# Performance work log

Measured on AMD Instinct MI355X. Metric: run time of the kernel, lower is better.

Reference implementation:

```python
import jax, jax.numpy as jnp
import numpy as np

N_TASK = 50000
N_PROC = 256
N_EDGES = 800000
EMB = 64
HEADS = 4
NLAYERS = 3
EDIM = 8
TDIM = 16
PDIM = 8
NGRAPHS = 8


def setup_inputs():
    key = jax.random.key(0)
    ks = jax.random.split(key, 30)

    def nrm(k, shape, fan_in):
        return jax.random.normal(k, shape, jnp.float32) / np.float32(np.sqrt(fan_in))

    inp = {}
    inp["x_task"] = jax.random.normal(ks[0], (N_TASK, TDIM), jnp.float32)
    inp["x_proc"] = jax.random.normal(ks[1], (N_PROC, PDIM), jnp.float32)
    inp["edge_index"] = jax.random.randint(ks[2], (2, N_EDGES), 0, N_TASK, dtype=jnp.int32)
    inp["edge_attr"] = jax.random.uniform(ks[3], (N_EDGES, EDIM), jnp.float32)
    inp["task_batch"] = jnp.sort(jax.random.randint(ks[4], (N_TASK,), 0, NGRAPHS, dtype=jnp.int32))
    inp["proc_batch"] = jnp.sort(jax.random.randint(ks[5], (N_PROC,), 0, NGRAPHS, dtype=jnp.int32))
    # input embeds
    inp["W_task"] = nrm(ks[6], (TDIM, EMB), TDIM)
    inp["b_task"] = jnp.zeros((EMB,), jnp.float32)
    inp["W_proc"] = nrm(ks[7], (PDIM, EMB), PDIM)
    inp["b_proc"] = jnp.zeros((EMB,), jnp.float32)
    # per-layer GAT params (stacked over layers)
    inp["gat_W"] = nrm(ks[8], (NLAYERS, EMB, HEADS * EMB), EMB)
    inp["gat_We"] = nrm(ks[9], (NLAYERS, EDIM, HEADS * EMB), EDIM)
    inp["att_src"] = nrm(ks[10], (NLAYERS, HEADS, EMB), EMB)
    inp["att_dst"] = nrm(ks[11], (NLAYERS, HEADS, EMB), EMB)
    inp["att_edge"] = nrm(ks[12], (NLAYERS, HEADS, EMB), EMB)
    inp["gat_b"] = jnp.zeros((NLAYERS, HEADS * EMB), jnp.float32)
    inp["proj_W"] = nrm(ks[13], (NLAYERS, HEADS * EMB, EMB), HEADS * EMB)
    inp["proj_b"] = jnp.zeros((NLAYERS, EMB), jnp.float32)
    inp["ln_g"] = jnp.ones((NLAYERS, EMB), jnp.float32)
    inp["ln_b"] = jnp.zeros((NLAYERS, EMB), jnp.float32)
    # heads
    inp["pt_W1"] = nrm(ks[14], (EMB, EMB // 2), EMB)
    inp["pt_b1"] = jnp.zeros((EMB // 2,), jnp.float32)
    inp["pt_W2"] = nrm(ks[15], (EMB // 2, 1), EMB // 2)
    inp["pt_b2"] = jnp.zeros((1,), jnp.float32)
    inp["v_W1"] = nrm(ks[16], (2 * EMB, EMB), 2 * EMB)
    inp["v_b1"] = jnp.zeros((EMB,), jnp.float32)
    inp["v_W2"] = nrm(ks[17], (EMB, 1), EMB)
    inp["v_b2"] = jnp.zeros((1,), jnp.float32)
    return inp


def _gat_layer(x, src, dst, eattr, W, We, a_s, a_d, a_e, bias):
    # PyG GATConv(in=-1 shared lin, heads=H, concat=True, edge_dim) with self loops already appended
    n = x.shape[0]
    xl = (x @ W).reshape(n, HEADS, EMB)            # [N,H,D]
    el = (eattr @ We).reshape(-1, HEADS, EMB)      # [E,H,D]
    a_src = jnp.einsum("nhd,hd->nh", xl, a_s)
    a_dst = jnp.einsum("nhd,hd->nh", xl, a_d)
    a_edg = jnp.einsum("ehd,hd->eh", el, a_e)
    alpha = jax.nn.leaky_relu(a_src[src] + a_dst[dst] + a_edg, 0.2)  # [E,H]
    m = jax.ops.segment_max(alpha, dst, num_segments=n)
    ex = jnp.exp(alpha - m[dst])
    denom = jax.ops.segment_sum(ex, dst, num_segments=n)
    coeff = ex / (denom[dst] + 1e-16)
    out = jax.ops.segment_sum(coeff[:, :, None] * xl[src], dst, num_segments=n)
    return out.reshape(n, HEADS * EMB) + bias


def _mean_pool(x, batch, g):
    s = jax.ops.segment_sum(x, batch, num_segments=g)
    cnt = jax.ops.segment_sum(jnp.ones((x.shape[0], 1), x.dtype), batch, num_segments=g)
    return s / jnp.maximum(cnt, 1.0)


def reference(x_task, x_proc, edge_attr, W_task, b_task, W_proc, b_proc, gat_W, gat_We,
              att_src, att_dst, att_edge, gat_b, proj_W, proj_b, ln_g, ln_b,
              pt_W1, pt_b1, pt_W2, pt_b2, v_W1, v_b1, v_W2, v_b2,
              edge_index, task_batch, proc_batch):
    h_t = x_task @ W_task + b_task
    h_p = x_proc @ W_proc + b_proc
    # add self loops; self-loop edge_attr = mean of edge_attr (PyG fill_value='mean')
    loop = jnp.arange(N_TASK, dtype=edge_index.dtype)
    src = jnp.concatenate([edge_index[0], loop])
    dst = jnp.concatenate([edge_index[1], loop])
    ea = jnp.concatenate([edge_attr, jnp.broadcast_to(edge_attr.mean(0), (N_TASK, EDIM))], axis=0)
    for l in range(NLAYERS):
        upd = _gat_layer(h_t, src, dst, ea, gat_W[l], gat_We[l], att_src[l], att_dst[l], att_edge[l], gat_b[l])
        upd = jax.nn.elu(upd @ proj_W[l] + proj_b[l])
        h = h_t + upd
        mu = h.mean(-1, keepdims=True)
        var = ((h - mu) ** 2).mean(-1, keepdims=True)
        h_t = (h - mu) / jnp.sqrt(var + 1e-5) * ln_g[l] + ln_b[l]
    task_logits = (jax.nn.relu(h_t @ pt_W1 + pt_b1) @ pt_W2 + pt_b2)[:, 0]
    tp = _mean_pool(h_t, task_batch, NGRAPHS)
    pp = _mean_pool(h_p, proc_batch, NGRAPHS)
    ge = jnp.concatenate([tp, pp], axis=1)
    value = jax.nn.relu(ge @ v_W1 + v_b1) @ v_W2 + v_b2
    return task_logits, value, h_t, h_p
```

## Files before the change

### kernel.cpp

```cpp
#include <hip/hip_runtime.h>
#include <hip/hip_bf16.h>
#include <math.h>

#define NT 50000
#define NP 256
#define NE 800000
#define ET 850000
#define EMBD 64
#define NHEADS 4
#define HE 256
#define NG 8

typedef __attribute__((ext_vector_type(8))) short bf16x8;
typedef __attribute__((ext_vector_type(4))) float f32x4;

#define OFF_DEG      0u
#define OFF_INDPTR   200192u
#define OFF_CURSOR   400384u
#define OFF_POS      600576u
#define OFF_SRCS     4000768u
#define OFF_MEAN     7400960u
#define OFF_M        7401216u
#define OFF_TPSUM    7401472u
#define OFF_TPCNT    7403520u
#define OFF_ASRC     7403776u
#define OFF_ADST     8204544u
#define OFF_AEDG     9805568u
#define OFF_HT       37005568u
#define OFF_HTB      49817856u
#define OFF_XL       56224000u
#define OFF_AGG      81824000u
#define OFF_WXF      107448576u
#define OFF_WPF      107546880u

__device__ __forceinline__ float bf_lo(unsigned int u) {
  union { unsigned int i; float f; } v; v.i = u << 16; return v.f;
}
__device__ __forceinline__ float bf_hi(unsigned int u) {
  union { unsigned int i; float f; } v; v.i = u & 0xffff0000u; return v.f;
}

__global__ __launch_bounds__(256) void k_embed_task(const float* __restrict__ x,
    const float* __restrict__ W, const float* __restrict__ b,
    float* __restrict__ ht, __hip_bfloat16* __restrict__ htb) {
  int lane = threadIdx.x & 63, wid = threadIdx.x >> 6;
  float breg[16];
  #pragma unroll
  for (int k = 0; k < 16; k++) breg[k] = W[k * 64 + lane];
  float bias = b[lane];
  int row0 = blockIdx.x * 64 + wid * 16;
  #pragma unroll 1
  for (int r = 0; r < 16; r++) {
    int row = row0 + r;
    if (row >= NT) return;
    const float4* xr = (const float4*)(x + (size_t)row * 16);
    float acc = bias;
    #pragma unroll
    for (int q = 0; q < 4; q++) {
      float4 v = xr[q];
      acc += v.x * breg[q*4+0] + v.y * breg[q*4+1] + v.z * breg[q*4+2] + v.w * breg[q*4+3];
    }
    ht[(size_t)row * 64 + lane] = acc;
    htb[(size_t)row * 64 + lane] = __float2bfloat16(acc);
  }
}

__global__ __launch_bounds__(256) void k_embed_proc(const float* __restrict__ x,
    const float* __restrict__ W, const float* __restrict__ b, float* __restrict__ hp) {
  int lane = threadIdx.x & 63, wid = threadIdx.x >> 6;
  float breg[8];
  #pragma unroll
  for (int k = 0; k < 8; k++) breg[k] = W[k * 64 + lane];
  float bias = b[lane];
  #pragma unroll 1
  for (int r = 0; r < 64; r++) {
    int row = wid * 64 + r;
    const float* xr = x + (size_t)row * 8;
    float acc = bias;
    #pragma unroll
    for (int k = 0; k < 8; k++) acc += xr[k] * breg[k];
    hp[(size_t)row * 64 + lane] = acc;
  }
}

__global__ __launch_bounds__(256) void k_edge_mean(const float* __restrict__ ea,
                                                   float* __restrict__ sums) {
  __shared__ float lds[256];
  int k = threadIdx.x & 7;
  int rlane = threadIdx.x >> 3;
  float s = 0.f;
  for (int row = blockIdx.x * 32 + rlane; row < NE; row += gridDim.x * 32)
    s += ea[(size_t)row * 8 + k];
  lds[threadIdx.x] = s;
  __syncthreads();
  for (int off = 128; off >= 8; off >>= 1) {
    if (threadIdx.x < off) lds[threadIdx.x] += lds[threadIdx.x + off];
    __syncthreads();
  }
  if (threadIdx.x < 8) atomicAdd(&sums[threadIdx.x], lds[threadIdx.x]);
}

__global__ __launch_bounds__(256) void k_degree(const int* __restrict__ ei1, int* __restrict__ deg) {
  int e = blockIdx.x * 256 + threadIdx.x;
  if (e >= ET) return;
  int d = (e < NE) ? ei1[e] : (e - NE);
  atomicAdd(&deg[d], 1);
}

__global__ __launch_bounds__(1024) void k_scan(const int* __restrict__ deg,
                                               int* __restrict__ indptr,
                                               int* __restrict__ cursor) {
  __shared__ int wsum[16];
  __shared__ int carry;
  int tid = threadIdx.x, lane = tid & 63, wid = tid >> 6;
  if (tid == 0) carry = 0;
  __syncthreads();
  for (int base = 0; base < NT; base += 1024) {
    int i = base + tid;
    int v = (i < NT) ? deg[i] : 0;
    int x = v;
    #pragma unroll
    for (int off = 1; off < 64; off <<= 1) {
      int t = __shfl_up(x, off, 64);
      if (lane >= off) x += t;
    }
    if (lane == 63) wsum[wid] = x;
    __syncthreads();
    int c0 = carry;
    if (wid == 0 && lane < 16) {
      int w = wsum[lane];
      #pragma unroll
      for (int off = 1; off < 16; off <<= 1) {
        int t = __shfl_up(w, off, 64);
        if (lane >= off) w += t;
      }
      wsum[lane] = w;
    }
    __syncthreads();
    int woff = (wid == 0) ? 0 : wsum[wid - 1];
    int incl = x + woff;
    if (i < NT) {
      int excl = c0 + incl - v;
      indptr[i] = excl;
      cursor[i] = excl;
    }
    __syncthreads();
    if (tid == 1023) carry = c0 + wsum[15];
    __syncthreads();
  }
  if (threadIdx.x == 0) indptr[NT] = carry;
}

__global__ __launch_bounds__(256) void k_fill(const int* __restrict__ ei0,
                                              const int* __restrict__ ei1,
                                              int* __restrict__ cursor,
                                              int* __restrict__ pos,
                                              int* __restrict__ srcs) {
  int e = blockIdx.x * 256 + threadIdx.x;
  if (e >= ET) return;
  int d, s;
  if (e < NE) { d = ei1[e]; s = ei0[e]; } else { d = e - NE; s = e - NE; }
  int p = atomicAdd(&cursor[d], 1);
  srcs[p] = s;
  pos[e] = p;
}

__global__ void k_prep_wx(const float* __restrict__ W, __hip_bfloat16* __restrict__ Wf) {
  int lane = threadIdx.x;
  int bid = blockIdx.x;
  int l = bid >> 5, rem = bid & 31, t = rem >> 1, kb = rem & 1;
  int quad = lane >> 4, l15 = lane & 15;
  const float* Wl = W + (size_t)l * 64 * 256;
  __hip_bfloat16* out = Wf + (size_t)l * 16384 + (size_t)((t * 2 + kb) * 64 + lane) * 8;
  #pragma unroll
  for (int j = 0; j < 8; j++)
    out[j] = __float2bfloat16(Wl[(kb * 32 + quad * 8 + j) * 256 + t * 16 + l15]);
}

__global__ void k_prep_wp(const float* __restrict__ W, __hip_bfloat16* __restrict__ Wf) {
  int lane = threadIdx.x;
  int bid = blockIdx.x;
  int l = bid >> 5, rem = bid & 31, t = rem >> 3, kb = rem & 7;
  int quad = lane >> 4, l15 = lane & 15;
  const float* Wl = W + (size_t)l * 256 * 64;
  __hip_bfloat16* out = Wf + (size_t)l * 16384 + (size_t)((t * 8 + kb) * 64 + lane) * 8;
  #pragma unroll
  for (int j = 0; j < 8; j++)
    out[j] = __float2bfloat16(Wl[(kb * 32 + quad * 8 + j) * 64 + t * 16 + l15]);
}

__global__ __launch_bounds__(256) void k_xl_mfma(
    const __hip_bfloat16* __restrict__ htb, const __hip_bfloat16* __restrict__ Wf,
    const float* __restrict__ as, const float* __restrict__ ad,
    __hip_bfloat16* __restrict__ xl, float* __restrict__ a_src, float* __restrict__ a_dst) {
  int lane = threadIdx.x & 63, wave = threadIdx.x >> 6;
  int quad = lane >> 4, l15 = lane & 15;
  int r0 = blockIdx.x * 64 + wave * 16;
  f32x4 acc[16];
  #pragma unroll
  for (int t = 0; t < 16; t++) acc[t] = (f32x4){0.f, 0.f, 0.f, 0.f};
  #pragma unroll
  for (int kb = 0; kb < 2; kb++) {
    bf16x8 a = *(const bf16x8*)(htb + (size_t)(r0 + l15) * 64 + kb * 32 + quad * 8);
    #pragma unroll
    for (int t = 0; t < 16; t++) {
      bf16x8 bfr = *(const bf16x8*)(Wf + (size_t)((t * 2 + kb) * 64 + lane) * 8);
      acc[t] = __builtin_amdgcn_mfma_f32_16x16x32_bf16(a, bfr, acc[t], 0, 0, 0);
    }
  }
  float asv[16], adv[16];
  #pragma unroll
  for (int t = 0; t < 16; t++) { asv[t] = as[t * 16 + l15]; adv[t] = ad[t * 16 + l15]; }
  #pragma unroll
  for (int reg = 0; reg < 4; reg++) {
    int row = r0 + quad * 4 + reg;
    bool ok = row < NT;
    float vs[4] = {0.f, 0.f, 0.f, 0.f}, vd[4] = {0.f, 0.f, 0.f, 0.f};
    #pragma unroll
    for (int t = 0; t < 16; t++) {
      float v = acc[t][reg];
      if (ok) xl[(size_t)row * HE + t * 16 + l15] = __float2bfloat16(v);
      vs[t >> 2] += v * asv[t];
      vd[t >> 2] += v * adv[t];
    }
    #pragma unroll
    for (int off = 8; off; off >>= 1) {
      #pragma unroll
      for (int h = 0; h < 4; h++) {
        vs[h] += __shfl_xor(vs[h], off, 64);
        vd[h] += __shfl_xor(vd[h], off, 64);
      }
    }
    if (ok && l15 == 0) {
      float4 s4; s4.x = vs[0]; s4.y = vs[1]; s4.z = vs[2]; s4.w = vs[3];
      float4 d4; d4.x = vd[0]; d4.y = vd[1]; d4.z = vd[2]; d4.w = vd[3];
      *(float4*)(a_src + (size_t)row * 4) = s4;
      *(float4*)(a_dst + (size_t)row * 4) = d4;
    }
  }
}

__global__ __launch_bounds__(256) void k_a_edg(const float* __restrict__ ea,
    const float* __restrict__ msum, const float* __restrict__ We,
    const float* __restrict__ ae, const int* __restrict__ pos,
    float* __restrict__ aedg_csr) {
  __shared__ float Ms[32];
  int t = threadIdx.x;
  if (t < 32) {
    int k = t >> 2, hh = t & 3;
    float s = 0.f;
    #pragma unroll
    for (int d = 0; d < 64; d++) s += We[k * HE + hh * 64 + d] * ae[hh * 64 + d];
    Ms[t] = s;
  }
  __syncthreads();
  int e = blockIdx.x * 256 + t;
  if (e >= ET) return;
  float v[8];
  if (e < NE) {
    const float4* p = (const float4*)(ea + (size_t)e * 8);
    float4 x0 = p[0], x1 = p[1];
    v[0] = x0.x; v[1] = x0.y; v[2] = x0.z; v[3] = x0.w;
    v[4] = x1.x; v[5] = x1.y; v[6] = x1.z; v[7] = x1.w;
  } else {
    #pragma unroll
    for (int k = 0; k < 8; k++) v[k] = msum[k] * (1.f / NE);
  }
  float rr[4];
  #pragma unroll
  for (int h = 0; h < 4; h++) {
    float s = 0.f;
    #pragma unroll
    for (int k = 0; k < 8; k++) s += v[k] * Ms[k * 4 + h];
    rr[h] = s;
  }
  float4 r; r.x = rr[0]; r.y = rr[1]; r.z = rr[2]; r.w = rr[3];
  *(float4*)(aedg_csr + (size_t)pos[e] * 4) = r;
}

__global__ __launch_bounds__(256) void k_attn(
    const __hip_bfloat16* __restrict__ xl, const float* __restrict__ a_src,
    const float* __restrict__ a_dst, const float* __restrict__ aedg_csr,
    const int* __restrict__ indptr, const int* __restrict__ srcs,
    const float* __restrict__ gb, __hip_bfloat16* __restrict__ agg) {
  int node = blockIdx.x * 4 + (threadIdx.x >> 6);
  int lane = threadIdx.x & 63;
  int h = lane >> 4;
  int hbase = lane & 48;
  int e15 = lane & 15;
  int beg = indptr[node], end = indptr[node + 1];
  float adh = a_dst[node * 4 + h];
  float M = -1e30f, S = 0.f;
  float acc0 = 0.f, acc1 = 0.f, acc2 = 0.f, acc3 = 0.f;
  for (int base = beg; base < end; base += 16) {
    int cnt = min(16, end - base);
    int el = base + e15;
    bool ok = e15 < cnt;
    int my_src = ok ? srcs[el] : 0;
    float aer = ok ? aedg_csr[(size_t)el * 4 + h] : 0.f;
    float asr = ok ? a_src[(size_t)my_src * 4 + h] : 0.f;
    float al = asr + adh + aer;
    al = (al > 0.f) ? al : 0.2f * al;
    if (!ok) al = -1e30f;
    float cm = al;
    #pragma unroll
    for (int off = 1; off < 16; off <<= 1) cm = fmaxf(cm, __shfl_xor(cm, off, 64));
    float newM = fmaxf(M, cm);
    float corr = __expf(M - newM);
    float ex = __expf(al - newM);
    float cs = ex;
    #pragma unroll
    for (int off = 1; off < 16; off <<= 1) cs += __shfl_xor(cs, off, 64);
    S = S * corr + cs;
    M = newM;
    acc0 *= corr; acc1 *= corr; acc2 *= corr; acc3 *= corr;
    if (cnt == 16) {
      #pragma unroll 4
      for (int j = 0; j < 16; j++) {
        int src = __shfl(my_src, j, 64);
        float cf = __shfl(ex, hbase | j, 64);
        uint2 u = *(const uint2*)(xl + (size_t)src * HE + lane * 4);
        acc0 += cf * bf_lo(u.x);
        acc1 += cf * bf_hi(u.x);
        acc2 += cf * bf_lo(u.y);
        acc3 += cf * bf_hi(u.y);
      }
    } else {
      for (int j = 0; j < cnt; j++) {
        int src = __shfl(my_src, j, 64);
        float cf = __shfl(ex, hbase | j, 64);
        uint2 u = *(const uint2*)(xl + (size_t)src * HE + lane * 4);
        acc0 += cf * bf_lo(u.x);
        acc1 += cf * bf_hi(u.x);
        acc2 += cf * bf_lo(u.y);
        acc3 += cf * bf_hi(u.y);
      }
    }
  }
  float inv = 1.f / (S + 1e-16f);
  float4 g4 = *(const float4*)(gb + lane * 4);
  unsigned int o0 = __bfloat16_as_ushort(__float2bfloat16(acc0 * inv + g4.x));
  unsigned int o1 = __bfloat16_as_ushort(__float2bfloat16(acc1 * inv + g4.y));
  unsigned int o2 = __bfloat16_as_ushort(__float2bfloat16(acc2 * inv + g4.z));
  unsigned int o3 = __bfloat16_as_ushort(__float2bfloat16(acc3 * inv + g4.w));
  uint2 out; out.x = o0 | (o1 << 16); out.y = o2 | (o3 << 16);
  *(uint2*)(agg + (size_t)node * HE + lane * 4) = out;
}

__global__ __launch_bounds__(256) void k_proj_mfma(
    const __hip_bfloat16* __restrict__ agg, const __hip_bfloat16* __restrict__ Wf,
    const float* __restrict__ pb, const float* __restrict__ g, const float* __restrict__ b,
    const float* __restrict__ ht_in, float* __restrict__ ht_out,
    __hip_bfloat16* __restrict__ htb_out, int writebf) {
  int lane = threadIdx.x & 63, wave = threadIdx.x >> 6;
  int quad = lane >> 4, l15 = lane & 15;
  int r0 = blockIdx.x * 64 + wave * 16;
  f32x4 acc[4];
  #pragma unroll
  for (int t = 0; t < 4; t++) acc[t] = (f32x4){0.f, 0.f, 0.f, 0.f};
  #pragma unroll
  for (int kb = 0; kb < 8; kb++) {
    bf16x8 a = *(const bf16x8*)(agg + (size_t)(r0 + l15) * HE + kb * 32 + quad * 8);
    #pragma unroll
    for (int t = 0; t < 4; t++) {
      bf16x8 bfr = *(const bf16x8*)(Wf + (size_t)((t * 8 + kb) * 64 + lane) * 8);
      acc[t] = __builtin_amdgcn_mfma_f32_16x16x32_bf16(a, bfr, acc[t], 0, 0, 0);
    }
  }
  float pbv[4], gv[4], bv[4];
  #pragma unroll
  for (int t = 0; t < 4; t++) {
    pbv[t] = pb[t * 16 + l15];
    gv[t] = g[t * 16 + l15];
    bv[t] = b[t * 16 + l15];
  }
  #pragma unroll
  for (int reg = 0; reg < 4; reg++) {
    int row = r0 + quad * 4 + reg;
    bool ok = row < NT;
    float h[4], rs = 0.f;
    #pragma unroll
    for (int t = 0; t < 4; t++) {
      float u = acc[t][reg] + pbv[t];
      u = (u > 0.f) ? u : (__expf(u) - 1.f);
      h[t] = ht_in[(size_t)row * 64 + t * 16 + l15] + u;
      rs += h[t];
    }
    #pragma unroll
    for (int off = 8; off; off >>= 1) rs += __shfl_xor(rs, off, 64);
    float mu = rs * 0.015625f;
    float vv = 0.f;
    #pragma unroll
    for (int t = 0; t < 4; t++) { float d = h[t] - mu; vv += d * d; }
    #pragma unroll
    for (int off = 8; off; off >>= 1) vv += __shfl_xor(vv, off, 64);
    float rstd = rsqrtf(vv * 0.015625f + 1e-5f);
    #pragma unroll
    for (int t = 0; t < 4; t++) {
      float o = (h[t] - mu) * rstd * gv[t] + bv[t];
      if (ok) {
        ht_out[(size_t)row * 64 + t * 16 + l15] = o;
        if (writebf) htb_out[(size_t)row * 64 + t * 16 + l15] = __float2bfloat16(o);
      }
    }
  }
}

__global__ __launch_bounds__(256) void k_task_head(const float* __restrict__ ht,
    const float* __restrict__ W1, const float* __restrict__ b1,
    const float* __restrict__ W2, const float* __restrict__ b2, float* __restrict__ logits) {
  __shared__ float lh[8 * 64];
  int t = threadIdx.x;
  size_t base = (size_t)blockIdx.x * 8 * 64;
  lh[t] = ht[base + t];
  lh[t + 256] = ht[base + t + 256];
  __syncthreads();
  int i = t >> 5, j = t & 31;
  float s = b1[j];
  #pragma unroll 8
  for (int d = 0; d < 64; d++) s += lh[i * 64 + d] * W1[d * 32 + j];
  s = fmaxf(s, 0.f);
  float p = s * W2[j];
  #pragma unroll
  for (int off = 16; off; off >>= 1) p += __shfl_xor(p, off, 64);
  if (j == 0) logits[blockIdx.x * 8 + i] = p + b2[0];
}

__global__ __launch_bounds__(256) void k_pool_task(const float* __restrict__ ht,
    const int* __restrict__ tb, float* __restrict__ sums, float* __restrict__ cnt) {
  int lane = threadIdx.x & 63, sub = threadIdx.x >> 6;
  float acc[8], c[8];
  #pragma unroll
  for (int g = 0; g < 8; g++) { acc[g] = 0.f; c[g] = 0.f; }
  int lim = min(NT, (int)((blockIdx.x + 1) * 512));
  for (int n = blockIdx.x * 512 + sub; n < lim; n += 4) {
    int g = tb[n];
    float v = ht[(size_t)n * 64 + lane];
    #pragma unroll
    for (int gg = 0; gg < 8; gg++) {
      if (g == gg) { acc[gg] += v; c[gg] += 1.f; }
    }
  }
  #pragma unroll
  for (int g = 0; g < 8; g++) {
    if (__any(acc[g] != 0.f || c[g] != 0.f)) {
      atomicAdd(&sums[g * 64 + lane], acc[g]);
      if (lane == 0) atomicAdd(&cnt[g], c[g]);
    }
  }
}

__global__ __launch_bounds__(512) void k_value(const float* __restrict__ tpsum,
    const float* __restrict__ tpcnt, const float* __restrict__ hp,
    const int* __restrict__ pbatch, const float* __restrict__ vW1,
    const float* __restrict__ vb1, const float* __restrict__ vW2,
    const float* __restrict__ vb2, float* __restrict__ val_out) {
  __shared__ float ge[8 * 128];
  int t = threadIdx.x;
  int g = t >> 6, d = t & 63;
  float c = fmaxf(tpcnt[g], 1.f);
  ge[g * 128 + d] = tpsum[g * 64 + d] / c;
  float s = 0.f, cc = 0.f;
  for (int p = 0; p < 256; p++) {
    int bg = pbatch[p];
    if (bg == g) { s += hp[(size_t)p * 64 + d]; cc += 1.f; }
  }
  ge[g * 128 + 64 + d] = s / fmaxf(cc, 1.f);
  __syncthreads();
  float acc = vb1[d];
  #pragma unroll 8
  for (int k = 0; k < 128; k++) acc += ge[g * 128 + k] * vW1[k * 64 + d];
  acc = fmaxf(acc, 0.f);
  float p = acc * vW2[d];
  #pragma unroll
  for (int off = 32; off; off >>= 1) p += __shfl_xor(p, off, 64);
  if (d == 0) val_out[g] = p + vb2[0];
}

extern "C" void kernel_launch(void* const* d_in, const int* in_sizes, int n_in,
                              void* d_out, int out_size, void* d_ws, size_t ws_size,
                              hipStream_t stream) {
  (void)in_sizes; (void)n_in; (void)out_size; (void)ws_size;
  const float* x_task  = (const float*)d_in[0];
  const float* x_proc  = (const float*)d_in[1];
  const int*   eidx    = (const int*)d_in[2];
  const float* eattr   = (const float*)d_in[3];
  const int*   tbatch  = (const int*)d_in[4];
  const int*   pbatch  = (const int*)d_in[5];
  const float* W_task  = (const float*)d_in[6];
  const float* b_task  = (const float*)d_in[7];
  const float* W_proc  = (const float*)d_in[8];
  const float* b_proc  = (const float*)d_in[9];
  const float* gat_W   = (const float*)d_in[10];
  const float* gat_We  = (const float*)d_in[11];
  const float* att_src = (const float*)d_in[12];
  const float* att_dst = (const float*)d_in[13];
  const float* att_edge= (const float*)d_in[14];
  const float* gat_b   = (const float*)d_in[15];
  const float* proj_W  = (const float*)d_in[16];
  const float* proj_b  = (const float*)d_in[17];
  const float* ln_g    = (const float*)d_in[18];
  const float* ln_b    = (const float*)d_in[19];
  const float* pt_W1   = (const float*)d_in[20];
  const float* pt_b1   = (const float*)d_in[21];
  const float* pt_W2   = (const float*)d_in[22];
  const float* pt_b2   = (const float*)d_in[23];
  const float* v_W1    = (const float*)d_in[24];
  const float* v_b1    = (const float*)d_in[25];
  const float* v_W2    = (const float*)d_in[26];
  const float* v_b2    = (const float*)d_in[27];

  char* ws = (char*)d_ws;
  int*   deg    = (int*)(ws + OFF_DEG);
  int*   indptr = (int*)(ws + OFF_INDPTR);
  int*   cursor = (int*)(ws + OFF_CURSOR);
  int*   pos    = (int*)(ws + OFF_POS);
  int*   srcs   = (int*)(ws + OFF_SRCS);
  float* msum   = (float*)(ws + OFF_MEAN);
  float* tpsum  = (float*)(ws + OFF_TPSUM);
  float* tpcnt  = (float*)(ws + OFF_TPCNT);
  float* a_src  = (float*)(ws + OFF_ASRC);
  float* a_dst  = (float*)(ws + OFF_ADST);
  float* a_edg  = (float*)(ws + OFF_AEDG);
  float* ht     = (float*)(ws + OFF_HT);
  __hip_bfloat16* htb = (__hip_bfloat16*)(ws + OFF_HTB);
  __hip_bfloat16* xl  = (__hip_bfloat16*)(ws + OFF_XL);
  __hip_bfloat16* agg = (__hip_bfloat16*)(ws + OFF_AGG);
  __hip_bfloat16* wxf = (__hip_bfloat16*)(ws + OFF_WXF);
  __hip_bfloat16* wpf = (__hip_bfloat16*)(ws + OFF_WPF);

  float* out_logits = (float*)d_out;
  float* out_value  = (float*)d_out + NT;
  float* out_ht     = (float*)d_out + NT + NG;
  float* out_hp     = (float*)d_out + NT + NG + (size_t)NT * EMBD;

  hipMemsetAsync(ws + OFF_DEG, 0, NT * 4, stream);
  hipMemsetAsync(ws + OFF_MEAN, 0, 2816, stream);

  k_embed_task<<<782, 256, 0, stream>>>(x_task, W_task, b_task, ht, htb);
  k_embed_proc<<<1, 256, 0, stream>>>(x_proc, W_proc, b_proc, out_hp);
  k_edge_mean<<<256, 256, 0, stream>>>(eattr, msum);
  k_degree<<<(ET + 255) / 256, 256, 0, stream>>>(eidx + NE, deg);
  k_scan<<<1, 1024, 0, stream>>>(deg, indptr, cursor);
  k_fill<<<(ET + 255) / 256, 256, 0, stream>>>(eidx, eidx + NE, cursor, pos, srcs);
  k_prep_wx<<<96, 64, 0, stream>>>(gat_W, wxf);
  k_prep_wp<<<96, 64, 0, stream>>>(proj_W, wpf);

  for (int l = 0; l < 3; l++) {
    k_xl_mfma<<<782, 256, 0, stream>>>(htb, wxf + (size_t)l * 16384,
                                       att_src + l * NHEADS * EMBD,
                                       att_dst + l * NHEADS * EMBD,
                                       xl, a_src, a_dst);
    k_a_edg<<<(ET + 255) / 256, 256, 0, stream>>>(eattr, msum,
                                                  gat_We + (size_t)l * 8 * HE,
                                                  att_edge + l * NHEADS * EMBD,
                                                  pos, a_edg);
    k_attn<<<NT / 4, 256, 0, stream>>>(xl, a_src, a_dst, a_edg, indptr, srcs,
                                       gat_b + l * HE, agg);
    float* htout = (l == 2) ? out_ht : ht;
    k_proj_mfma<<<782, 256, 0, stream>>>(agg, wpf + (size_t)l * 16384,
                                         proj_b + l * EMBD, ln_g + l * EMBD,
                                         ln_b + l * EMBD, ht, htout, htb,
                                         (l == 2) ? 0 : 1);
  }

  k_task_head<<<NT / 8, 256, 0, stream>>>(out_ht, pt_W1, pt_b1, pt_W2, pt_b2, out_logits);
  k_pool_task<<<(NT + 511) / 512, 256, 0, stream>>>(out_ht, tbatch, tpsum, tpcnt);
  k_value<<<1, 512, 0, stream>>>(tpsum, tpcnt, out_hp, pbatch, v_W1, v_b1, v_W2, v_b2, out_value);
}
```

Before: 768.6 us.

## Fuse edge-attention term into attn kernel and parallelize CSR scan

Drops the per-layer edge-logit kernel. Attention now reads raw edge attributes via a CSR record holding edge id and source, and dots them with a precomputed per-layer 8x4 projection. The single-block serial prefix scan is replaced by a two-pass multi-block scan. Degree counting and the edge mean are fused, the weight prep kernels are merged, and proc embedding moves into the value kernel. This removes launches and a scattered write pass, in exchange for random 32-byte edge-attribute gathers inside attention.

Result: faster. 720.5 us (-6.3%).

```diff
diff --git a/kernel.cpp b/kernel.cpp
--- a/kernel.cpp
+++ b/kernel.cpp
@@ -10,28 +10,29 @@
 #define NHEADS 4
 #define HE 256
 #define NG 8
+#define NBLK 49
 
 typedef __attribute__((ext_vector_type(8))) short bf16x8;
 typedef __attribute__((ext_vector_type(4))) float f32x4;
 
-#define OFF_DEG      0u
-#define OFF_INDPTR   200192u
-#define OFF_CURSOR   400384u
-#define OFF_POS      600576u
-#define OFF_SRCS     4000768u
-#define OFF_MEAN     7400960u
-#define OFF_M        7401216u
-#define OFF_TPSUM    7401472u
-#define OFF_TPCNT    7403520u
-#define OFF_ASRC     7403776u
-#define OFF_ADST     8204544u
-#define OFF_AEDG     9805568u
-#define OFF_HT       37005568u
-#define OFF_HTB      49817856u
-#define OFF_XL       56224000u
-#define OFF_AGG      81824000u
-#define OFF_WXF      107448576u
-#define OFF_WPF      107546880u
+#define OFF_DEG    0u
+#define OFF_INDPTR 200192u
+#define OFF_CURSOR 400384u
+#define OFF_BLKSUM 600576u
+#define OFF_MG     600832u
+#define OFF_MH     601216u
+#define OFF_MEAN   601280u
+#define OFF_TPSUM  601344u
+#define OFF_TPCNT  603392u
+#define OFF_ER     603648u
+#define OFF_ASRC   7403648u
+#define OFF_ADST   8204416u
+#define OFF_HT     9005184u
+#define OFF_HTB    21817472u
+#define OFF_XL     28223616u
+#define OFF_AGG    53823616u
+#define OFF_WXF    79448192u
+#define OFF_WPF    79546496u
 
 __device__ __forceinline__ float bf_lo(unsigned int u) {
   union { unsigned int i; float f; } v; v.i = u << 16; return v.f;
@@ -65,128 +66,135 @@
   }
 }
 
-__global__ __launch_bounds__(256) void k_embed_proc(const float* __restrict__ x,
-    const float* __restrict__ W, const float* __restrict__ b, float* __restrict__ hp) {
-  int lane = threadIdx.x & 63, wid = threadIdx.x >> 6;
-  float breg[8];
-  #pragma unroll
-  for (int k = 0; k < 8; k++) breg[k] = W[k * 64 + lane];
-  float bias = b[lane];
-  #pragma unroll 1
-  for (int r = 0; r < 64; r++) {
-    int row = wid * 64 + r;
-    const float* xr = x + (size_t)row * 8;
-    float acc = bias;
-    #pragma unroll
-    for (int k = 0; k < 8; k++) acc += xr[k] * breg[k];
-    hp[(size_t)row * 64 + lane] = acc;
-  }
-}
-
-__global__ __launch_bounds__(256) void k_edge_mean(const float* __restrict__ ea,
-                                                   float* __restrict__ sums) {
+__global__ __launch_bounds__(256) void k_degree_mean(const int* __restrict__ ei1,
+    const float* __restrict__ ea, int* __restrict__ deg, float* __restrict__ sums) {
   __shared__ float lds[256];
-  int k = threadIdx.x & 7;
-  int rlane = threadIdx.x >> 3;
+  int tid = threadIdx.x;
+  int e = blockIdx.x * 256 + tid;
+  if (e < ET) {
+    int d = (e < NE) ? ei1[e] : (e - NE);
+    atomicAdd(&deg[d], 1);
+  }
+  int k = tid & 7, rl = tid >> 3;
   float s = 0.f;
-  for (int row = blockIdx.x * 32 + rlane; row < NE; row += gridDim.x * 32)
+  for (int row = blockIdx.x * 32 + rl; row < NE; row += gridDim.x * 32)
     s += ea[(size_t)row * 8 + k];
-  lds[threadIdx.x] = s;
+  lds[tid] = s;
   __syncthreads();
   for (int off = 128; off >= 8; off >>= 1) {
-    if (threadIdx.x < off) lds[threadIdx.x] += lds[threadIdx.x + off];
+    if (tid < off) lds[tid] += lds[tid + off];
     __syncthreads();
   }
-  if (threadIdx.x < 8) atomicAdd(&sums[threadIdx.x], lds[threadIdx.x]);
-}
-
-__global__ __launch_bounds__(256) void k_degree(const int* __restrict__ ei1, int* __restrict__ deg) {
-  int e = blockIdx.x * 256 + threadIdx.x;
-  if (e >= ET) return;
-  int d = (e < NE) ? ei1[e] : (e - NE);
-  atomicAdd(&deg[d], 1);
-}
-
-__global__ __launch_bounds__(1024) void k_scan(const int* __restrict__ deg,
-                                               int* __restrict__ indptr,
-                                               int* __restrict__ cursor) {
+  if (tid < 8) atomicAdd(&sums[tid], lds[tid]);
+}
+
+__global__ __launch_bounds__(1024) void k_scanA(const int* __restrict__ deg,
+    int* __restrict__ indptr, int* __restrict__ blksum) {
   __shared__ int wsum[16];
-  __shared__ int carry;
   int tid = threadIdx.x, lane = tid & 63, wid = tid >> 6;
-  if (tid == 0) carry = 0;
-  __syncthreads();
-  for (int base = 0; base < NT; base += 1024) {
-    int i = base + tid;
-    int v = (i < NT) ? deg[i] : 0;
-    int x = v;
-    #pragma unroll
-    for (int off = 1; off < 64; off <<= 1) {
-      int t = __shfl_up(x, off, 64);
-      if (lane >= off) x += t;
-    }
-    if (lane == 63) wsum[wid] = x;
-    __syncthreads();
-    int c0 = carry;
-    if (wid == 0 && lane < 16) {
-      int w = wsum[lane];
-      #pragma unroll
-      for (int off = 1; off < 16; off <<= 1) {
-        int t = __shfl_up(w, off, 64);
-        if (lane >= off) w += t;
-      }
-      wsum[lane] = w;
-    }
-    __syncthreads();
-    int woff = (wid == 0) ? 0 : wsum[wid - 1];
-    int incl = x + woff;
-    if (i < NT) {
-      int excl = c0 + incl - v;
-      indptr[i] = excl;
-      cursor[i] = excl;
-    }
-    __syncthreads();
-    if (tid == 1023) carry = c0 + wsum[15];
-    __syncthreads();
-  }
-  if (threadIdx.x == 0) indptr[NT] = carry;
+  int i = blockIdx.x * 1024 + tid;
+  int v = (i < NT) ? deg[i] : 0;
+  int x = v;
+  #pragma unroll
+  for (int off = 1; off < 64; off <<= 1) {
+    int t = __shfl_up(x, off, 64);
+    if (lane >= off) x += t;
+  }
+  if (lane == 63) wsum[wid] = x;
+  __syncthreads();
+  if (wid == 0 && lane < 16) {
+    int w = wsum[lane];
+    #pragma unroll
+    for (int off = 1; off < 16; off <<= 1) {
+      int t = __shfl_up(w, off, 64);
+      if (lane >= off) w += t;
+    }
+    wsum[lane] = w;
+  }
+  __syncthreads();
+  int woff = (wid == 0) ? 0 : wsum[wid - 1];
+  if (i < NT) indptr[i] = x + woff - v;
+  if (tid == 1023) blksum[blockIdx.x] = wsum[15];
+}
+
+__global__ __launch_bounds__(1024) void k_scanB(const int* __restrict__ blksum,
+    int* __restrict__ indptr, int* __restrict__ cursor) {
+  __shared__ int bs[NBLK];
+  int tid = threadIdx.x;
+  if (tid < NBLK) bs[tid] = blksum[tid];
+  __syncthreads();
+  int off = 0;
+  for (int j = 0; j < (int)blockIdx.x; j++) off += bs[j];
+  int i = blockIdx.x * 1024 + tid;
+  if (i < NT) {
+    int e = indptr[i] + off;
+    indptr[i] = e;
+    cursor[i] = e;
+  }
+  if (blockIdx.x == 0 && tid == 0) {
+    int tot = 0;
+    for (int j = 0; j < NBLK; j++) tot += bs[j];
+    indptr[NT] = tot;
+  }
 }
 
 __global__ __launch_bounds__(256) void k_fill(const int* __restrict__ ei0,
                                               const int* __restrict__ ei1,
                                               int* __restrict__ cursor,
-                                              int* __restrict__ pos,
-                                              int* __restrict__ srcs) {
+                                              uint2* __restrict__ er) {
   int e = blockIdx.x * 256 + threadIdx.x;
   if (e >= ET) return;
   int d, s;
   if (e < NE) { d = ei1[e]; s = ei0[e]; } else { d = e - NE; s = e - NE; }
   int p = atomicAdd(&cursor[d], 1);
-  srcs[p] = s;
-  pos[e] = p;
-}
-
-__global__ void k_prep_wx(const float* __restrict__ W, __hip_bfloat16* __restrict__ Wf) {
+  uint2 r; r.x = (unsigned)e; r.y = (unsigned)s;
+  er[p] = r;
+}
+
+__global__ __launch_bounds__(128) void k_mprep(const float* __restrict__ We,
+    const float* __restrict__ ae, const float* __restrict__ msum,
+    float* __restrict__ Mg, float* __restrict__ Mh) {
+  int t = threadIdx.x;
+  if (t < 96) {
+    int l = t >> 5, idx = t & 31, k = idx >> 2, h = idx & 3;
+    const float* Wl = We + (size_t)l * 8 * HE;
+    const float* al = ae + (size_t)l * NHEADS * EMBD;
+    float s = 0.f;
+    #pragma unroll
+    for (int d = 0; d < 64; d++) s += Wl[k * HE + h * 64 + d] * al[h * 64 + d];
+    Mg[t] = s;
+  }
+  __syncthreads();
+  if (t < 12) {
+    int l = t >> 2, h = t & 3;
+    float m = 0.f;
+    #pragma unroll
+    for (int k = 0; k < 8; k++) m += msum[k] * (1.f / NE) * Mg[l * 32 + k * 4 + h];
+    Mh[t] = m;
+  }
+}
+
+__global__ void k_prep_w(const float* __restrict__ Wx, const float* __restrict__ Wp,
+                         __hip_bfloat16* __restrict__ Wxf, __hip_bfloat16* __restrict__ Wpf) {
   int lane = threadIdx.x;
   int bid = blockIdx.x;
-  int l = bid >> 5, rem = bid & 31, t = rem >> 1, kb = rem & 1;
   int quad = lane >> 4, l15 = lane & 15;
-  const float* Wl = W + (size_t)l * 64 * 256;
-  __hip_bfloat16* out = Wf + (size_t)l * 16384 + (size_t)((t * 2 + kb) * 64 + lane) * 8;
-  #pragma unroll
-  for (int j = 0; j < 8; j++)
-    out[j] = __float2bfloat16(Wl[(kb * 32 + quad * 8 + j) * 256 + t * 16 + l15]);
-}
-
-__global__ void k_prep_wp(const float* __restrict__ W, __hip_bfloat16* __restrict__ Wf) {
-  int lane = threadIdx.x;
-  int bid = blockIdx.x;
-  int l = bid >> 5, rem = bid & 31, t = rem >> 3, kb = rem & 7;
-  int quad = lane >> 4, l15 = lane & 15;
-  const float* Wl = W + (size_t)l * 256 * 64;
-  __hip_bfloat16* out = Wf + (size_t)l * 16384 + (size_t)((t * 8 + kb) * 64 + lane) * 8;
-  #pragma unroll
-  for (int j = 0; j < 8; j++)
-    out[j] = __float2bfloat16(Wl[(kb * 32 + quad * 8 + j) * 64 + t * 16 + l15]);
+  if (bid < 96) {
+    int l = bid >> 5, rem = bid & 31, t = rem >> 1, kb = rem & 1;
+    const float* Wl = Wx + (size_t)l * 64 * 256;
+    __hip_bfloat16* out = Wxf + (size_t)l * 16384 + (size_t)((t * 2 + kb) * 64 + lane) * 8;
+    #pragma unroll
+    for (int j = 0; j < 8; j++)
+      out[j] = __float2bfloat16(Wl[(kb * 32 + quad * 8 + j) * 256 + t * 16 + l15]);
+  } else {
+    bid -= 96;
+    int l = bid >> 5, rem = bid & 31, t = rem >> 3, kb = rem & 7;
+    const float* Wl = Wp + (size_t)l * 256 * 64;
+    __hip_bfloat16* out = Wpf + (size_t)l * 16384 + (size_t)((t * 8 + kb) * 64 + lane) * 8;
+    #pragma unroll
+    for (int j = 0; j < 8; j++)
+      out[j] = __float2bfloat16(Wl[(kb * 32 + quad * 8 + j) * 64 + t * 16 + l15]);
+  }
 }
 
 __global__ __launch_bounds__(256) void k_xl_mfma(
@@ -240,54 +248,21 @@
   }
 }
 
-__global__ __launch_bounds__(256) void k_a_edg(const float* __restrict__ ea,
-    const float* __restrict__ msum, const float* __restrict__ We,
-    const float* __restrict__ ae, const int* __restrict__ pos,
-    float* __restrict__ aedg_csr) {
-  __shared__ float Ms[32];
-  int t = threadIdx.x;
-  if (t < 32) {
-    int k = t >> 2, hh = t & 3;
-    float s = 0.f;
-    #pragma unroll
-    for (int d = 0; d < 64; d++) s += We[k * HE + hh * 64 + d] * ae[hh * 64 + d];
-    Ms[t] = s;
-  }
-  __syncthreads();
-  int e = blockIdx.x * 256 + t;
-  if (e >= ET) return;
-  float v[8];
-  if (e < NE) {
-    const float4* p = (const float4*)(ea + (size_t)e * 8);
-    float4 x0 = p[0], x1 = p[1];
-    v[0] = x0.x; v[1] = x0.y; v[2] = x0.z; v[3] = x0.w;
-    v[4] = x1.x; v[5] = x1.y; v[6] = x1.z; v[7] = x1.w;
-  } else {
-    #pragma unroll
-    for (int k = 0; k < 8; k++) v[k] = msum[k] * (1.f / NE);
-  }
-  float rr[4];
-  #pragma unroll
-  for (int h = 0; h < 4; h++) {
-    float s = 0.f;
-    #pragma unroll
-    for (int k = 0; k < 8; k++) s += v[k] * Ms[k * 4 + h];
-    rr[h] = s;
-  }
-  float4 r; r.x = rr[0]; r.y = rr[1]; r.z = rr[2]; r.w = rr[3];
-  *(float4*)(aedg_csr + (size_t)pos[e] * 4) = r;
-}
-
 __global__ __launch_bounds__(256) void k_attn(
     const __hip_bfloat16* __restrict__ xl, const float* __restrict__ a_src,
-    const float* __restrict__ a_dst, const float* __restrict__ aedg_csr,
-    const int* __restrict__ indptr, const int* __restrict__ srcs,
+    const float* __restrict__ a_dst, const float* __restrict__ ea,
+    const uint2* __restrict__ er, const int* __restrict__ indptr,
+    const float* __restrict__ Mg, const float* __restrict__ Mh,
     const float* __restrict__ gb, __hip_bfloat16* __restrict__ agg) {
   int node = blockIdx.x * 4 + (threadIdx.x >> 6);
   int lane = threadIdx.x & 63;
   int h = lane >> 4;
   int hbase = lane & 48;
   int e15 = lane & 15;
+  float MsR[8];
+  #pragma unroll
+  for (int k = 0; k < 8; k++) MsR[k] = Mg[k * 4 + h];
+  float mhR = Mh[h];
   int beg = indptr[node], end = indptr[node + 1];
   float adh = a_dst[node * 4 + h];
   float M = -1e30f, S = 0.f;
@@ -296,10 +271,20 @@
     int cnt = min(16, end - base);
     int el = base + e15;
     bool ok = e15 < cnt;
-    int my_src = ok ? srcs[el] : 0;
-    float aer = ok ? aedg_csr[(size_t)el * 4 + h] : 0.f;
+    uint2 r = ok ? er[el] : (uint2){0u, 0u};
+    int e = (int)r.x;
+    int my_src = (int)r.y;
     float asr = ok ? a_src[(size_t)my_src * 4 + h] : 0.f;
-    float al = asr + adh + aer;
+    float aeh;
+    if (e < NE) {
+      const float4* p = (const float4*)(ea + (size_t)e * 8);
+      float4 v0 = p[0], v1 = p[1];
+      aeh = v0.x * MsR[0] + v0.y * MsR[1] + v0.z * MsR[2] + v0.w * MsR[3]
+          + v1.x * MsR[4] + v1.y * MsR[5] + v1.z * MsR[6] + v1.w * MsR[7];
+    } else {
+      aeh = mhR;
+    }
+    float al = asr + adh + aeh;
     al = (al > 0.f) ? al : 0.2f * al;
     if (!ok) al = -1e30f;
     float cm = al;
@@ -451,19 +436,33 @@
 }
 
 __global__ __launch_bounds__(512) void k_value(const float* __restrict__ tpsum,
-    const float* __restrict__ tpcnt, const float* __restrict__ hp,
-    const int* __restrict__ pbatch, const float* __restrict__ vW1,
-    const float* __restrict__ vb1, const float* __restrict__ vW2,
-    const float* __restrict__ vb2, float* __restrict__ val_out) {
+    const float* __restrict__ tpcnt, const float* __restrict__ x_proc,
+    const float* __restrict__ W_proc, const float* __restrict__ b_proc,
+    float* __restrict__ hp_out, const int* __restrict__ pbatch,
+    const float* __restrict__ vW1, const float* __restrict__ vb1,
+    const float* __restrict__ vW2, const float* __restrict__ vb2,
+    float* __restrict__ val_out) {
   __shared__ float ge[8 * 128];
   int t = threadIdx.x;
   int g = t >> 6, d = t & 63;
+  float wreg[8];
+  #pragma unroll
+  for (int k = 0; k < 8; k++) wreg[k] = W_proc[k * 64 + d];
+  float bd = b_proc[d];
+  for (int p = g; p < 256; p += 8) {
+    const float* xr = x_proc + (size_t)p * 8;
+    float a = bd;
+    #pragma unroll
+    for (int k = 0; k < 8; k++) a += xr[k] * wreg[k];
+    hp_out[(size_t)p * 64 + d] = a;
+  }
+  __syncthreads();
   float c = fmaxf(tpcnt[g], 1.f);
   ge[g * 128 + d] = tpsum[g * 64 + d] / c;
   float s = 0.f, cc = 0.f;
   for (int p = 0; p < 256; p++) {
     int bg = pbatch[p];
-    if (bg == g) { s += hp[(size_t)p * 64 + d]; cc += 1.f; }
+    if (bg == g) { s += hp_out[(size_t)p * 64 + d]; cc += 1.f; }
   }
   ge[g * 128 + 64 + d] = s / fmaxf(cc, 1.f);
   __syncthreads();
@@ -514,14 +513,15 @@
   int*   deg    = (int*)(ws + OFF_DEG);
   int*   indptr = (int*)(ws + OFF_INDPTR);
   int*   cursor = (int*)(ws + OFF_CURSOR);
-  int*   pos    = (int*)(ws + OFF_POS);
-  int*   srcs   = (int*)(ws + OFF_SRCS);
+  int*   blksum = (int*)(ws + OFF_BLKSUM);
+  float* Mg     = (float*)(ws + OFF_MG);
+  float* Mh     = (float*)(ws + OFF_MH);
   float* msum   = (float*)(ws + OFF_MEAN);
   float* tpsum  = (float*)(ws + OFF_TPSUM);
   float* tpcnt  = (float*)(ws + OFF_TPCNT);
+  uint2* er     = (uint2*)(ws + OFF_ER);
   float* a_src  = (float*)(ws + OFF_ASRC);
   float* a_dst  = (float*)(ws + OFF_ADST);
-  float* a_edg  = (float*)(ws + OFF_AEDG);
   float* ht     = (float*)(ws + OFF_HT);
   __hip_bfloat16* htb = (__hip_bfloat16*)(ws + OFF_HTB);
   __hip_bfloat16* xl  = (__hip_bfloat16*)(ws + OFF_XL);
@@ -535,27 +535,23 @@
   float* out_hp     = (float*)d_out + NT + NG + (size_t)NT * EMBD;
 
   hipMemsetAsync(ws + OFF_DEG, 0, NT * 4, stream);
-  hipMemsetAsync(ws + OFF_MEAN, 0, 2816, stream);
+  hipMemsetAsync(ws + OFF_MEAN, 0, 2144, stream);
 
   k_embed_task<<<782, 256, 0, stream>>>(x_task, W_task, b_task, ht, htb);
-  k_embed_proc<<<1, 256, 0, stream>>>(x_proc, W_proc, b_proc, out_hp);
-  k_edge_mean<<<256, 256, 0, stream>>>(eattr, msum);
-  k_degree<<<(ET + 255) / 256, 256, 0, stream>>>(eidx + NE, deg);
-  k_scan<<<1, 1024, 0, stream>>>(deg, indptr, cursor);
-  k_fill<<<(ET + 255) / 256, 256, 0, stream>>>(eidx, eidx + NE, cursor, pos, srcs);
-  k_prep_wx<<<96, 64, 0, stream>>>(gat_W, wxf);
-  k_prep_wp<<<96, 64, 0, stream>>>(proj_W, wpf);
+  k_degree_mean<<<(ET + 255) / 256, 256, 0, stream>>>(eidx + NE, eattr, deg, msum);
+  k_scanA<<<NBLK, 1024, 0, stream>>>(deg, indptr, blksum);
+  k_scanB<<<NBLK, 1024, 0, stream>>>(blksum, indptr, cursor);
+  k_mprep<<<1, 128, 0, stream>>>(gat_We, att_edge, msum, Mg, Mh);
+  k_fill<<<(ET + 255) / 256, 256, 0, stream>>>(eidx, eidx + NE, cursor, er);
+  k_prep_w<<<192, 64, 0, stream>>>(gat_W, proj_W, wxf, wpf);
 
   for (int l = 0; l < 3; l++) {
     k_xl_mfma<<<782, 256, 0, stream>>>(htb, wxf + (size_t)l * 16384,
                                        att_src + l * NHEADS * EMBD,
                                        att_dst + l * NHEADS * EMBD,
                                        xl, a_src, a_dst);
-    k_a_edg<<<(ET + 255) / 256, 256, 0, stream>>>(eattr, msum,
-                                                  gat_We + (size_t)l * 8 * HE,
-                                                  att_edge + l * NHEADS * EMBD,
-                                                  pos, a_edg);
-    k_attn<<<NT / 4, 256, 0, stream>>>(xl, a_src, a_dst, a_edg, indptr, srcs,
+    k_attn<<<NT / 4, 256, 0, stream>>>(xl, a_src, a_dst, eattr, er, indptr,
+                                       Mg + l * 32, Mh + l * 4,
                                        gat_b + l * HE, agg);
     float* htout = (l == 2) ? out_ht : ht;
     k_proj_mfma<<<782, 256, 0, stream>>>(agg, wpf + (size_t)l * 16384,
@@ -566,5 +562,6 @@
 
   k_task_head<<<NT / 8, 256, 0, stream>>>(out_ht, pt_W1, pt_b1, pt_W2, pt_b2, out_logits);
   k_pool_task<<<(NT + 511) / 512, 256, 0, stream>>>(out_ht, tbatch, tpsum, tpcnt);
-  k_value<<<1, 512, 0, stream>>>(tpsum, tpcnt, out_hp, pbatch, v_W1, v_b1, v_W2, v_b2, out_value);
-}
+  k_value<<<1, 512, 0, stream>>>(tpsum, tpcnt, x_proc, W_proc, b_proc, out_hp,
+                                 pbatch, v_W1, v_b1, v_W2, v_b2, out_value);
+}
```
